# Performance work log

Measured on AMD Instinct MI355X. Metric: run time of the kernel, lower is better.

## Reference

```python
import jax, jax.numpy as jnp
import numpy as np

BITS = 4            # bits per quantized weight
NPACK = 8           # 32-bit container / 4-bit values
CBITS = 32          # compression dtype bit width (int32)
GROUP = 128         # quantization group size along in_features
IN = 4096
OUT = 11008
BATCH = 32


def _dequant(packed_weight, scale):
    # Unpack signed int4 values: (p << (32 - 4*(e+1))) >> 28, arithmetic shift
    # sign-extends, matching the torch recover() path for weight_dtype=int8.
    e = jnp.arange(NPACK, dtype=jnp.int32)                      # [8]
    shifted = (packed_weight[:, :, None] << (CBITS - BITS * (e + 1))) >> (CBITS - BITS)  # [O, I/8, 8]
    w_int = shifted.reshape(OUT, IN).astype(jnp.int8)           # signed int4 in int8
    # Per-group scale: reshape to [O*I/GROUP, GROUP] * [O*I/GROUP, 1]
    w = w_int.astype(jnp.float32).reshape(-1, GROUP) * scale.reshape(-1, 1)
    return w.reshape(OUT, IN)


def setup_inputs() -> dict:
    key = jax.random.key(0)
    k1, k2, k3, k4 = jax.random.split(key, 4)
    x = jax.random.normal(k1, (BATCH, IN), dtype=jnp.float32)
    packed_weight = jax.random.randint(
        k2, (OUT, IN // NPACK), jnp.iinfo(jnp.int32).min, jnp.iinfo(jnp.int32).max,
        dtype=jnp.int32)
    scale = jax.random.uniform(k3, (OUT, IN // GROUP), dtype=jnp.float32,
                               minval=0.001, maxval=0.02)
    bias = jax.random.normal(k4, (OUT,), dtype=jnp.float32)
    return {"x": x, "packed_weight": packed_weight, "scale": scale, "bias": bias}


def reference(x, packed_weight, scale, bias):
    W = _dequant(packed_weight, scale)      # [OUT, IN] fp32
    return x @ W.T + bias                    # F.linear(x, W, bias)
```

## Files before the change

kernel.cpp:

```cpp
#include <hip/hip_runtime.h>

#define IN_F   4096
#define OUT_F  11008
#define BATCH  32
#define NG     32
#define PACKS  512
#define SLICES 16
#define SLICE_F (BATCH * OUT_F)

typedef __bf16 bf16x8_t __attribute__((ext_vector_type(8)));
typedef float  floatx4_t __attribute__((ext_vector_type(4)));

__global__ __launch_bounds__(256) void prep_x(const float* __restrict__ x,
                                              unsigned short* __restrict__ xp) {
  int c  = blockIdx.x * 256 + threadIdx.x;
  int mm = c & 31;
  int k0 = ((c >> 5) & 3) * 32 + ((c >> 7) & 3) * 8 + (c >> 9) * 128;
  const float* src = x + mm * IN_F + k0;
  float4 f0 = *(const float4*)(src);
  float4 f1 = *(const float4*)(src + 4);
  float v[8] = {f0.x, f0.y, f0.z, f0.w, f1.x, f1.y, f1.z, f1.w};
  union { unsigned short s[8]; uint4 u; } r;
#pragma unroll
  for (int j = 0; j < 8; ++j) {
    unsigned int u = __float_as_uint(v[j]);
    unsigned int rnd = ((u >> 16) & 1u) + 0x7fffu;
    r.s[j] = (unsigned short)((u + rnd) >> 16);
  }
  *(uint4*)(xp + c * 8) = r.u;
}

__device__ inline bf16x8_t unpack8(int p) {
  union { unsigned short u[8]; bf16x8_t v; } r;
#pragma unroll
  for (int j = 0; j < 8; ++j) {
    int nib = (p << (28 - 4 * j)) >> 28;
    float f = (float)nib;
    r.u[j] = (unsigned short)(__float_as_uint(f) >> 16);
  }
  return r.v;
}

__device__ inline bf16x8_t load_frag(const unsigned short* p) {
  union { uint4 u; bf16x8_t v; } x;
  x.u = *(const uint4*)p;
  return x.v;
}

__global__ __launch_bounds__(256) void wql_part(
    const int* __restrict__ pw, const float* __restrict__ scale,
    const unsigned short* __restrict__ xp, float* __restrict__ part) {
  const int tid = threadIdx.x;
  const int l   = tid & 63;
  const int w   = tid >> 6;
  const int col = l & 15;
  const int q   = l >> 4;
  const int n0  = blockIdx.x * 32;
  const int kc  = blockIdx.y;
  const int nA  = n0 + col;
  const int nB  = n0 + 16 + col;

  floatx4_t acc00 = {0.f, 0.f, 0.f, 0.f};
  floatx4_t acc01 = {0.f, 0.f, 0.f, 0.f};
  floatx4_t acc10 = {0.f, 0.f, 0.f, 0.f};
  floatx4_t acc11 = {0.f, 0.f, 0.f, 0.f};

  const int g0 = kc * 8 + w * 2;
#pragma unroll 1
  for (int gi = 0; gi < 2; ++gi) {
    const int gg = g0 + gi;
    int4 pA = *(const int4*)(pw + nA * PACKS + gg * 16 + q * 4);
    int4 pB = *(const int4*)(pw + nB * PACKS + gg * 16 + q * 4);
    float sA = scale[nA * NG + gg];
    float sB = scale[nB * NG + gg];

    const unsigned short* ab = xp + (gg * 512 + q * 32 + col) * 8;
    bf16x8_t a0[4], a1[4];
#pragma unroll
    for (int t = 0; t < 4; ++t) {
      a0[t] = load_frag(ab + t * 1024);
      a1[t] = load_frag(ab + t * 1024 + 128);
    }

    floatx4_t t00 = {0.f, 0.f, 0.f, 0.f};
    floatx4_t t01 = {0.f, 0.f, 0.f, 0.f};
    floatx4_t t10 = {0.f, 0.f, 0.f, 0.f};
    floatx4_t t11 = {0.f, 0.f, 0.f, 0.f};
    int pAv[4] = {pA.x, pA.y, pA.z, pA.w};
    int pBv[4] = {pB.x, pB.y, pB.z, pB.w};
#pragma unroll
    for (int t = 0; t < 4; ++t) {
      bf16x8_t b0 = unpack8(pAv[t]);
      bf16x8_t b1 = unpack8(pBv[t]);
      t00 = __builtin_amdgcn_mfma_f32_16x16x32_bf16(a0[t], b0, t00, 0, 0, 0);
      t10 = __builtin_amdgcn_mfma_f32_16x16x32_bf16(a1[t], b0, t10, 0, 0, 0);
      t01 = __builtin_amdgcn_mfma_f32_16x16x32_bf16(a0[t], b1, t01, 0, 0, 0);
      t11 = __builtin_amdgcn_mfma_f32_16x16x32_bf16(a1[t], b1, t11, 0, 0, 0);
    }
#pragma unroll
    for (int r = 0; r < 4; ++r) {
      acc00[r] += t00[r] * sA;
      acc10[r] += t10[r] * sA;
      acc01[r] += t01[r] * sB;
      acc11[r] += t11[r] * sB;
    }
  }

  float* wsp = part + (kc * 4 + w) * SLICE_F + n0;
#pragma unroll
  for (int r = 0; r < 4; ++r) {
    int row = q * 4 + r;
    wsp[row * OUT_F + col]             = acc00[r];
    wsp[row * OUT_F + 16 + col]        = acc01[r];
    wsp[(16 + row) * OUT_F + col]      = acc10[r];
    wsp[(16 + row) * OUT_F + 16 + col] = acc11[r];
  }
}

__global__ __launch_bounds__(256) void reduce_out(
    const float* __restrict__ part, const float* __restrict__ bias,
    float* __restrict__ out) {
  int e4 = blockIdx.x * 256 + threadIdx.x;
  int e  = e4 << 2;
  int o  = e % OUT_F;
  float4 s = *(const float4*)(bias + o);
#pragma unroll
  for (int k = 0; k < SLICES; ++k) {
    float4 p = *(const float4*)(part + k * SLICE_F + e);
    s.x += p.x; s.y += p.y; s.z += p.z; s.w += p.w;
  }
  *(float4*)(out + e) = s;
}

extern "C" void kernel_launch(void* const* d_in, const int* in_sizes, int n_in,
                              void* d_out, int out_size, void* d_ws, size_t ws_size,
                              hipStream_t stream) {
  const float* x     = (const float*)d_in[0];
  const int*   pw    = (const int*)d_in[1];
  const float* scale = (const float*)d_in[2];
  const float* bias  = (const float*)d_in[3];
  float* out = (float*)d_out;
  unsigned short* xp = (unsigned short*)d_ws;
  float* part = (float*)((char*)d_ws + (1 << 20));

  hipLaunchKernelGGL(prep_x, dim3(16384 / 256), dim3(256), 0, stream, x, xp);
  hipLaunchKernelGGL(wql_part, dim3(OUT_F / 32, 4), dim3(256), 0, stream,
                     pw, scale, xp, part);
  hipLaunchKernelGGL(reduce_out, dim3(BATCH * OUT_F / 4 / 256), dim3(256), 0,
                     stream, part, bias, out);
}
```

Baseline: 89.05 us.

## Reduce per-wave partials in LDS to cut split-K workspace traffic

Blocks now use 8 waves of 512 threads, each wave handling one quantization group, instead of 4 waves that each loop over two groups. The eight per-wave partial tiles are summed in shared memory before a single store, so the split-K workspace drops from 16 slices to 4. This cuts global write traffic in the GEMM kernel and read traffic in the reduce kernel. In exchange it adds a block-wide barrier, needs LDS storage, and doubles the block size, which may limit occupancy.

```diff
diff --git a/kernel.cpp b/kernel.cpp
--- a/kernel.cpp
+++ b/kernel.cpp
@@ -5,7 +5,7 @@
 #define BATCH  32
 #define NG     32
 #define PACKS  512
-#define SLICES 16
+#define SLICES 4
 #define SLICE_F (BATCH * OUT_F)
 
 typedef __bf16 bf16x8_t __attribute__((ext_vector_type(8)));
@@ -47,9 +47,11 @@
   return x.v;
 }
 
-__global__ __launch_bounds__(256) void wql_part(
+__global__ __launch_bounds__(512) void wql_part(
     const int* __restrict__ pw, const float* __restrict__ scale,
     const unsigned short* __restrict__ xp, float* __restrict__ part) {
+  __shared__ float lds[8][BATCH * 32];
+
   const int tid = threadIdx.x;
   const int l   = tid & 63;
   const int w   = tid >> 6;
@@ -59,61 +61,53 @@
   const int kc  = blockIdx.y;
   const int nA  = n0 + col;
   const int nB  = n0 + 16 + col;
+  const int gg  = kc * 8 + w;
 
-  floatx4_t acc00 = {0.f, 0.f, 0.f, 0.f};
-  floatx4_t acc01 = {0.f, 0.f, 0.f, 0.f};
-  floatx4_t acc10 = {0.f, 0.f, 0.f, 0.f};
-  floatx4_t acc11 = {0.f, 0.f, 0.f, 0.f};
+  int4 pA = *(const int4*)(pw + nA * PACKS + gg * 16 + q * 4);
+  int4 pB = *(const int4*)(pw + nB * PACKS + gg * 16 + q * 4);
+  float sA = scale[nA * NG + gg];
+  float sB = scale[nB * NG + gg];
 
-  const int g0 = kc * 8 + w * 2;
-#pragma unroll 1
-  for (int gi = 0; gi < 2; ++gi) {
-    const int gg = g0 + gi;
-    int4 pA = *(const int4*)(pw + nA * PACKS + gg * 16 + q * 4);
-    int4 pB = *(const int4*)(pw + nB * PACKS + gg * 16 + q * 4);
-    float sA = scale[nA * NG + gg];
-    float sB = scale[nB * NG + gg];
-
-    const unsigned short* ab = xp + (gg * 512 + q * 32 + col) * 8;
-    bf16x8_t a0[4], a1[4];
+  const unsigned short* ab = xp + (gg * 512 + q * 32 + col) * 8;
+  bf16x8_t a0[4], a1[4];
 #pragma unroll
-    for (int t = 0; t < 4; ++t) {
-      a0[t] = load_frag(ab + t * 1024);
-      a1[t] = load_frag(ab + t * 1024 + 128);
-    }
-
-    floatx4_t t00 = {0.f, 0.f, 0.f, 0.f};
-    floatx4_t t01 = {0.f, 0.f, 0.f, 0.f};
-    floatx4_t t10 = {0.f, 0.f, 0.f, 0.f};
-    floatx4_t t11 = {0.f, 0.f, 0.f, 0.f};
-    int pAv[4] = {pA.x, pA.y, pA.z, pA.w};
-    int pBv[4] = {pB.x, pB.y, pB.z, pB.w};
-#pragma unroll
-    for (int t = 0; t < 4; ++t) {
-      bf16x8_t b0 = unpack8(pAv[t]);
-      bf16x8_t b1 = unpack8(pBv[t]);
-      t00 = __builtin_amdgcn_mfma_f32_16x16x32_bf16(a0[t], b0, t00, 0, 0, 0);
-      t10 = __builtin_amdgcn_mfma_f32_16x16x32_bf16(a1[t], b0, t10, 0, 0, 0);
-      t01 = __builtin_amdgcn_mfma_f32_16x16x32_bf16(a0[t], b1, t01, 0, 0, 0);
-      t11 = __builtin_amdgcn_mfma_f32_16x16x32_bf16(a1[t], b1, t11, 0, 0, 0);
-    }
-#pragma unroll
-    for (int r = 0; r < 4; ++r) {
-      acc00[r] += t00[r] * sA;
-      acc10[r] += t10[r] * sA;
-      acc01[r] += t01[r] * sB;
-      acc11[r] += t11[r] * sB;
-    }
+  for (int t = 0; t < 4; ++t) {
+    a0[t] = load_frag(ab + t * 1024);
+    a1[t] = load_frag(ab + t * 1024 + 128);
   }
 
-  float* wsp = part + (kc * 4 + w) * SLICE_F + n0;
+  floatx4_t t00 = {0.f, 0.f, 0.f, 0.f};
+  floatx4_t t01 = {0.f, 0.f, 0.f, 0.f};
+  floatx4_t t10 = {0.f, 0.f, 0.f, 0.f};
+  floatx4_t t11 = {0.f, 0.f, 0.f, 0.f};
+  int pAv[4] = {pA.x, pA.y, pA.z, pA.w};
+  int pBv[4] = {pB.x, pB.y, pB.z, pB.w};
+#pragma unroll
+  for (int t = 0; t < 4; ++t) {
+    bf16x8_t b0 = unpack8(pAv[t]);
+    bf16x8_t b1 = unpack8(pBv[t]);
+    t00 = __builtin_amdgcn_mfma_f32_16x16x32_bf16(a0[t], b0, t00, 0, 0, 0);
+    t10 = __builtin_amdgcn_mfma_f32_16x16x32_bf16(a1[t], b0, t10, 0, 0, 0);
+    t01 = __builtin_amdgcn_mfma_f32_16x16x32_bf16(a0[t], b1, t01, 0, 0, 0);
+    t11 = __builtin_amdgcn_mfma_f32_16x16x32_bf16(a1[t], b1, t11, 0, 0, 0);
+  }
+
 #pragma unroll
   for (int r = 0; r < 4; ++r) {
     int row = q * 4 + r;
-    wsp[row * OUT_F + col]             = acc00[r];
-    wsp[row * OUT_F + 16 + col]        = acc01[r];
-    wsp[(16 + row) * OUT_F + col]      = acc10[r];
-    wsp[(16 + row) * OUT_F + 16 + col] = acc11[r];
+    lds[w][row * 32 + col]             = t00[r] * sA;
+    lds[w][row * 32 + 16 + col]        = t01[r] * sB;
+    lds[w][(16 + row) * 32 + col]      = t10[r] * sA;
+    lds[w][(16 + row) * 32 + 16 + col] = t11[r] * sB;
+  }
+  __syncthreads();
+
+  float* wsp = part + kc * SLICE_F + n0;
+  for (int e = tid; e < BATCH * 32; e += 512) {
+    int row = e >> 5, cl = e & 31;
+    float s = lds[0][e] + lds[1][e] + lds[2][e] + lds[3][e]
+            + lds[4][e] + lds[5][e] + lds[6][e] + lds[7][e];
+    wsp[row * OUT_F + cl] = s;
   }
 }
 
@@ -144,7 +138,7 @@
   float* part = (float*)((char*)d_ws + (1 << 20));
 
   hipLaunchKernelGGL(prep_x, dim3(16384 / 256), dim3(256), 0, stream, x, xp);
-  hipLaunchKernelGGL(wql_part, dim3(OUT_F / 32, 4), dim3(256), 0, stream,
+  hipLaunchKernelGGL(wql_part, dim3(OUT_F / 32, 4), dim3(512), 0, stream,
                      pw, scale, xp, part);
   hipLaunchKernelGGL(reduce_out, dim3(BATCH * OUT_F / 4 / 256), dim3(256), 0,
                      stream, part, bias, out);
```

After: 85.11 us. 4.4% less time.
